# Kernel optimization log

Hardware: AMD Instinct MI355X
Metric: run time of the kernel (lower is better)

Reference implementation:

```python
import jax, jax.numpy as jnp
import numpy as np

N = 50000
T = 6
E = 800000
F_IN = 64
HID = 64
HEADS = 4
NEG_SLOPE = 0.2
BN_EPS = 1e-5


def _gat_layer(x, src, dst, W, att_src, att_dst, bias, concat):
    # x: [N, Fin]; W: [Fin, H*C]; att_*: [H, C]; src/dst: [E+N] (self loops appended)
    n = x.shape[0]
    H, C = att_src.shape
    xl = (x @ W).reshape(n, H, C)                     # [N, H, C]
    a_src = jnp.sum(xl * att_src[None], axis=-1)      # [N, H]
    a_dst = jnp.sum(xl * att_dst[None], axis=-1)      # [N, H]
    e = jax.nn.leaky_relu(a_src[src] + a_dst[dst], NEG_SLOPE)  # [E', H]
    # segment softmax over destination nodes (every node has a self loop)
    m = jax.ops.segment_max(e, dst, num_segments=n)
    ex = jnp.exp(e - m[dst])
    s = jax.ops.segment_sum(ex, dst, num_segments=n)
    alpha = ex / (s[dst] + 1e-16)                     # [E', H]
    msg = alpha[:, :, None] * xl[src]                 # [E', H, C]
    out = jax.ops.segment_sum(msg, dst, num_segments=n)  # [N, H, C]
    if concat:
        out = out.reshape(n, H * C)
    else:
        out = out.mean(axis=1)
    return out + bias


def _forward(x_seq, edge_index, W1, as1, ad1, b1, W2, as2, ad2, b2,
             cw1, cb1, g1, be1, cw2, cb2, g2, be2, lw1, lb1, lw2, lb2):
    n = x_seq.shape[1]
    self_loop = jnp.arange(n, dtype=edge_index.dtype)
    src = jnp.concatenate([edge_index[0], self_loop])
    dst = jnp.concatenate([edge_index[1], self_loop])

    def per_t(x):
        h = _gat_layer(x, src, dst, W1, as1, ad1, b1, concat=True)
        h = jax.nn.elu(h)
        h = _gat_layer(h, src, dst, W2, as2, ad2, b2, concat=False)
        h = jax.nn.elu(h)
        return h                                      # [N, HID]

    temporal = jax.vmap(per_t)(x_seq)                 # [T, N, HID]
    temporal = jnp.transpose(temporal, (1, 2, 0))     # [N, HID, T]

    def conv_bn_relu(t, cw, cb, g, be):
        y = jax.lax.conv_general_dilated(
            t, cw, window_strides=(1,), padding=[(1, 1)],
            dimension_numbers=('NCH', 'OIH', 'NCH')) + cb[None, :, None]
        # BatchNorm1d in eval mode, running_mean=0, running_var=1
        y = y * (g / jnp.sqrt(1.0 + BN_EPS))[None, :, None] + be[None, :, None]
        return jax.nn.relu(y)

    t = conv_bn_relu(temporal, cw1, cb1, g1, be1)
    t = conv_bn_relu(t, cw2, cb2, g2, be2)
    pooled = t.mean(axis=-1)                          # adaptive avg pool -> [N, HID]
    h = jax.nn.relu(pooled @ lw1 + lb1)
    logits = h @ lw2 + lb2                            # [N, 1]
    return logits


def setup_inputs() -> dict:
    key = jax.random.key(0)
    ks = jax.random.split(key, 20)
    C1 = HID // HEADS  # 16
    s = 0.1
    return {
        'x_seq': jax.random.normal(ks[0], (T, N, F_IN), jnp.float32),
        'edge_index': jax.random.randint(ks[1], (2, E), 0, N, jnp.int32),
        'W1': jax.random.normal(ks[2], (F_IN, HEADS * C1), jnp.float32) * s,
        'as1': jax.random.normal(ks[3], (HEADS, C1), jnp.float32) * s,
        'ad1': jax.random.normal(ks[4], (HEADS, C1), jnp.float32) * s,
        'b1': jnp.zeros((HEADS * C1,), jnp.float32),
        'W2': jax.random.normal(ks[5], (HID, HEADS * HID), jnp.float32) * s,
        'as2': jax.random.normal(ks[6], (HEADS, HID), jnp.float32) * s,
        'ad2': jax.random.normal(ks[7], (HEADS, HID), jnp.float32) * s,
        'b2': jnp.zeros((HID,), jnp.float32),
        'cw1': jax.random.normal(ks[8], (HID, HID, 3), jnp.float32) * s,
        'cb1': jnp.zeros((HID,), jnp.float32),
        'g1': jnp.ones((HID,), jnp.float32),
        'be1': jnp.zeros((HID,), jnp.float32),
        'cw2': jax.random.normal(ks[9], (HID, HID, 3), jnp.float32) * s,
        'cb2': jnp.zeros((HID,), jnp.float32),
        'g2': jnp.ones((HID,), jnp.float32),
        'be2': jnp.zeros((HID,), jnp.float32),
        'lw1': jax.random.normal(ks[10], (HID, HID // 2), jnp.float32) * s,
        'lb1': jnp.zeros((HID // 2,), jnp.float32),
        'lw2': jax.random.normal(ks[11], (HID // 2, 1), jnp.float32) * s,
        'lb2': jnp.zeros((1,), jnp.float32),
    }


def reference(x_seq, edge_index, W1, as1, ad1, b1, W2, as2, ad2, b2,
              cw1, cb1, g1, be1, cw2, cb2, g2, be2, lw1, lb1, lw2, lb2):
    return _forward(x_seq, edge_index, W1, as1, ad1, b1, W2, as2, ad2, b2,
                    cw1, cb1, g1, be1, cw2, cb2, g2, be2, lw1, lb1, lw2, lb2)
```

## Files before the change

kernel.cpp:

```cpp
#include <hip/hip_runtime.h>
#include <math.h>

#define NN 50000
#define EE 800000
#define TT 6

__device__ __forceinline__ float lrelu(float x){ return x > 0.f ? x : 0.2f*x; }
__device__ __forceinline__ float eluf(float x){ return x > 0.f ? x : expm1f(x); }

__global__ void k_init_counts(int* __restrict__ c){
  int i = blockIdx.x*256 + threadIdx.x;
  if (i < NN) c[i] = 1;
}

__global__ void k_hist(const int* __restrict__ dst, int* __restrict__ c){
  int i = blockIdx.x*256 + threadIdx.x;
  if (i < EE) atomicAdd(&c[dst[i]], 1);
}

__global__ void k_scanA(const int* __restrict__ cnt, int* __restrict__ excl,
                        int* __restrict__ bsum){
  __shared__ int sh[1024];
  int tid = threadIdx.x;
  int i = blockIdx.x*1024 + tid;
  int v = (i < NN) ? cnt[i] : 0;
  int x = v;
  sh[tid] = x; __syncthreads();
  for (int off = 1; off < 1024; off <<= 1){
    int y = (tid >= off) ? sh[tid - off] : 0;
    __syncthreads();
    x += y; sh[tid] = x; __syncthreads();
  }
  if (i < NN) excl[i] = x - v;
  if (tid == 1023) bsum[blockIdx.x] = x;
}

__global__ void k_scanB(int* __restrict__ bsum, int nb){
  if (threadIdx.x == 0){
    int run = 0;
    for (int b = 0; b < nb; ++b){ int t = bsum[b]; bsum[b] = run; run += t; }
  }
}

__global__ void k_scanC(const int* __restrict__ excl, const int* __restrict__ bsum,
                        int* __restrict__ rowptr, int* __restrict__ cursor){
  int i = blockIdx.x*1024 + threadIdx.x;
  if (i < NN){
    int v = excl[i] + bsum[blockIdx.x];
    rowptr[i] = v; cursor[i] = v;
  }
  if (i == 0) rowptr[NN] = EE + NN;
}

__global__ void k_scatter(const int* __restrict__ ei, int* __restrict__ cursor,
                          int* __restrict__ csr){
  int i = blockIdx.x*256 + threadIdx.x;
  if (i < EE){
    int d = ei[EE + i];
    int p = atomicAdd(&cursor[d], 1);
    csr[p] = ei[i];
  } else if (i < EE + NN){
    int v = i - EE;
    int p = atomicAdd(&cursor[v], 1);
    csr[p] = v;
  }
}

__global__ void k_prep(const float* __restrict__ W1, const float* __restrict__ as1,
                       const float* __restrict__ ad1,
                       const float* __restrict__ W2, const float* __restrict__ as2,
                       const float* __restrict__ ad2,
                       const float* __restrict__ cw1, const float* __restrict__ cw2,
                       const float* __restrict__ lw1,
                       float* __restrict__ Was1, float* __restrict__ Wad1,
                       float* __restrict__ Wat2, float* __restrict__ Wb,
                       float4* __restrict__ wq1, float4* __restrict__ wq2,
                       float* __restrict__ lw1t){
  int tid = threadIdx.x;
  int k = tid >> 2, h = tid & 3;
  float s1 = 0.f, d1 = 0.f, s2 = 0.f, d2 = 0.f;
  for (int c = 0; c < 16; ++c){
    float w = W1[k*64 + h*16 + c];
    s1 += w * as1[h*16 + c];
    d1 += w * ad1[h*16 + c];
  }
  for (int c = 0; c < 64; ++c){
    float w = W2[k*256 + h*64 + c];
    s2 += w * as2[h*64 + c];
    d2 += w * ad2[h*64 + c];
  }
  Was1[k*4+h] = s1; Wad1[k*4+h] = d1;
  Wat2[k*8 + h] = s2; Wat2[k*8 + 4 + h] = d2;
  for (int idx = tid; idx < 256*64; idx += 256){
    int kf = idx >> 6, c = idx & 63;
    int hh = kf >> 6, kk = kf & 63;
    Wb[idx] = W2[kk*256 + hh*64 + c];
  }
  for (int idx = tid; idx < 64*64; idx += 256){
    int o = idx >> 6, i = idx & 63;
    wq1[idx] = make_float4(cw1[o*192+i*3], cw1[o*192+i*3+1], cw1[o*192+i*3+2], 0.f);
    wq2[idx] = make_float4(cw2[o*192+i*3], cw2[o*192+i*3+1], cw2[o*192+i*3+2], 0.f);
  }
  for (int idx = tid; idx < 32*64; idx += 256){
    int j = idx >> 6, kk = idx & 63;
    lw1t[idx] = lw1[kk*32 + j];
  }
}

__global__ __launch_bounds__(256) void k_gemm_att1(const float* __restrict__ A,
                            const float* __restrict__ W,
                            const float* __restrict__ Was, const float* __restrict__ Wad,
                            float* __restrict__ Xl, float* __restrict__ a_src,
                            float* __restrict__ a_dst){
  __shared__ float At[64][16];
  int tid = threadIdx.x;
  int r0 = blockIdx.x * 16;
  {
    const float4* A4 = (const float4*)(A + (size_t)r0*64);
    float4 v = A4[tid];
    int r = tid >> 4, k4 = (tid & 15) << 2;
    At[k4+0][r] = v.x; At[k4+1][r] = v.y;
    At[k4+2][r] = v.z; At[k4+3][r] = v.w;
  }
  __syncthreads();
  int col = tid & 63;
  int rbase = (tid >> 6) << 2;
  float acc0=0.f, acc1=0.f, acc2=0.f, acc3=0.f;
  for (int k = 0; k < 64; ++k){
    float w = W[k*64 + col];
    float4 a4 = *(const float4*)&At[k][rbase];
    acc0 += a4.x*w; acc1 += a4.y*w; acc2 += a4.z*w; acc3 += a4.w*w;
  }
  Xl[(size_t)(r0+rbase+0)*64 + col] = acc0;
  Xl[(size_t)(r0+rbase+1)*64 + col] = acc1;
  Xl[(size_t)(r0+rbase+2)*64 + col] = acc2;
  Xl[(size_t)(r0+rbase+3)*64 + col] = acc3;
  if (tid < 128){
    int r = tid >> 3, jx = tid & 7;
    int h = jx & 3;
    const float* Wv = (jx < 4) ? Was : Wad;
    float a = 0.f;
    for (int k = 0; k < 64; ++k) a += At[k][r] * Wv[k*4 + h];
    if (jx < 4) a_src[(r0 + r)*4 + h] = a;
    else        a_dst[(r0 + r)*4 + h] = a;
  }
}

__global__ void k_agg1(const float* __restrict__ xl, const float* __restrict__ a_src,
                       const float* __restrict__ a_dst, const float* __restrict__ b1,
                       const float* __restrict__ Wat2,
                       const int* __restrict__ rowptr, const int* __restrict__ csr,
                       float* __restrict__ h1,
                       float* __restrict__ a_src2, float* __restrict__ a_dst2){
  int lane = threadIdx.x & 63;
  int wid  = threadIdx.x >> 6;
  int n = blockIdx.x*4 + wid;
  int h = lane >> 4;
  float ad = a_dst[n*4 + h];
  int rs = rowptr[n], re = rowptr[n+1];
  float s = 0.f, acc = 0.f;
  int j = rs;
  for (; j + 4 <= re; j += 4){
    int sn0=csr[j], sn1=csr[j+1], sn2=csr[j+2], sn3=csr[j+3];
    float e0=a_src[sn0*4+h], e1=a_src[sn1*4+h], e2=a_src[sn2*4+h], e3=a_src[sn3*4+h];
    float x0=xl[(size_t)sn0*64+lane], x1=xl[(size_t)sn1*64+lane];
    float x2=xl[(size_t)sn2*64+lane], x3=xl[(size_t)sn3*64+lane];
    float p0=__expf(lrelu(e0+ad)), p1=__expf(lrelu(e1+ad));
    float p2=__expf(lrelu(e2+ad)), p3=__expf(lrelu(e3+ad));
    s += p0; acc += p0*x0;
    s += p1; acc += p1*x1;
    s += p2; acc += p2*x2;
    s += p3; acc += p3*x3;
  }
  for (; j < re; ++j){
    int sn = csr[j];
    float p = __expf(lrelu(a_src[sn*4+h] + ad));
    float x = xl[(size_t)sn*64 + lane];
    s += p; acc += p*x;
  }
  float hv = eluf(acc/(s + 1e-16f) + b1[lane]);
  h1[(size_t)n*64 + lane] = hv;
  float4 wA = ((const float4*)Wat2)[lane*2];
  float4 wB = ((const float4*)Wat2)[lane*2 + 1];
  float p[8];
  p[0]=hv*wA.x; p[1]=hv*wA.y; p[2]=hv*wA.z; p[3]=hv*wA.w;
  p[4]=hv*wB.x; p[5]=hv*wB.y; p[6]=hv*wB.z; p[7]=hv*wB.w;
#pragma unroll
  for (int off = 32; off >= 1; off >>= 1){
#pragma unroll
    for (int q = 0; q < 8; ++q) p[q] += __shfl_xor(p[q], off);
  }
  if (lane == 0){
    ((float4*)a_src2)[n] = make_float4(p[0],p[1],p[2],p[3]);
    ((float4*)a_dst2)[n] = make_float4(p[4],p[5],p[6],p[7]);
  }
}

__global__ void k_agg2(const float* __restrict__ h1, const float* __restrict__ a_src,
                       const float* __restrict__ a_dst,
                       const int* __restrict__ rowptr, const int* __restrict__ csr,
                       float* __restrict__ agg){
  int lane = threadIdx.x & 63;
  int wid  = threadIdx.x >> 6;
  int n = blockIdx.x*4 + wid;
  float4 ad = ((const float4*)a_dst)[n];
  int rs = rowptr[n], re = rowptr[n+1];
  float s0=0.f,s1=0.f,s2=0.f,s3=0.f;
  float g0=0.f,g1=0.f,g2=0.f,g3=0.f;
  int j = rs;
  for (; j + 4 <= re; j += 4){
    int sa=csr[j], sb=csr[j+1], sc=csr[j+2], sd=csr[j+3];
    float4 ea = ((const float4*)a_src)[sa];
    float4 eb = ((const float4*)a_src)[sb];
    float4 ec = ((const float4*)a_src)[sc];
    float4 ed = ((const float4*)a_src)[sd];
    float xa = h1[(size_t)sa*64 + lane];
    float xb = h1[(size_t)sb*64 + lane];
    float xc = h1[(size_t)sc*64 + lane];
    float xd = h1[(size_t)sd*64 + lane];
    float pa0=__expf(lrelu(ea.x+ad.x)), pa1=__expf(lrelu(ea.y+ad.y));
    float pa2=__expf(lrelu(ea.z+ad.z)), pa3=__expf(lrelu(ea.w+ad.w));
    float pb0=__expf(lrelu(eb.x+ad.x)), pb1=__expf(lrelu(eb.y+ad.y));
    float pb2=__expf(lrelu(eb.z+ad.z)), pb3=__expf(lrelu(eb.w+ad.w));
    float pc0=__expf(lrelu(ec.x+ad.x)), pc1=__expf(lrelu(ec.y+ad.y));
    float pc2=__expf(lrelu(ec.z+ad.z)), pc3=__expf(lrelu(ec.w+ad.w));
    float pd0=__expf(lrelu(ed.x+ad.x)), pd1=__expf(lrelu(ed.y+ad.y));
    float pd2=__expf(lrelu(ed.z+ad.z)), pd3=__expf(lrelu(ed.w+ad.w));
    s0 += pa0+pb0+pc0+pd0; g0 += pa0*xa + pb0*xb + pc0*xc + pd0*xd;
    s1 += pa1+pb1+pc1+pd1; g1 += pa1*xa + pb1*xb + pc1*xc + pd1*xd;
    s2 += pa2+pb2+pc2+pd2; g2 += pa2*xa + pb2*xb + pc2*xc + pd2*xd;
    s3 += pa3+pb3+pc3+pd3; g3 += pa3*xa + pb3*xb + pc3*xc + pd3*xd;
  }
  for (; j < re; ++j){
    int sn = csr[j];
    float4 ev = ((const float4*)a_src)[sn];
    float x = h1[(size_t)sn*64 + lane];
    float p0=__expf(lrelu(ev.x+ad.x)), p1=__expf(lrelu(ev.y+ad.y));
    float p2=__expf(lrelu(ev.z+ad.z)), p3=__expf(lrelu(ev.w+ad.w));
    s0 += p0; g0 += p0*x;
    s1 += p1; g1 += p1*x;
    s2 += p2; g2 += p2*x;
    s3 += p3; g3 += p3*x;
  }
  size_t base = (size_t)n*256 + lane;
  agg[base      ] = g0/(s0 + 1e-16f);
  agg[base +  64] = g1/(s1 + 1e-16f);
  agg[base + 128] = g2/(s2 + 1e-16f);
  agg[base + 192] = g3/(s3 + 1e-16f);
}

__global__ __launch_bounds__(256) void k_out2(const float* __restrict__ agg,
                                              const float* __restrict__ Wb,
                                              const float* __restrict__ b2,
                                              float* __restrict__ Xq, int t){
  __shared__ float AtF[256*20];
  int tid = threadIdx.x;
  int r0 = blockIdx.x * 16;
  const float4* A4 = (const float4*)(agg + (size_t)r0*256);
#pragma unroll
  for (int jj = 0; jj < 4; ++jj){
    int m = tid + 256*jj;
    float4 v = A4[m];
    int row = m >> 6, k0 = (m & 63) << 2;
    AtF[(k0+0)*20 + row] = v.x;
    AtF[(k0+1)*20 + row] = v.y;
    AtF[(k0+2)*20 + row] = v.z;
    AtF[(k0+3)*20 + row] = v.w;
  }
  __syncthreads();
  int col = tid & 63;
  int rbase = (tid >> 6) << 2;
  float acc0=0.f, acc1=0.f, acc2=0.f, acc3=0.f;
  for (int k = 0; k < 256; ++k){
    float w = Wb[(size_t)k*64 + col];
    float4 a4 = *(const float4*)&AtF[k*20 + rbase];
    acc0 += a4.x*w; acc1 += a4.y*w; acc2 += a4.z*w; acc3 += a4.w*w;
  }
  float bb = b2[col];
  float4 v = make_float4(eluf(0.25f*acc0 + bb), eluf(0.25f*acc1 + bb),
                         eluf(0.25f*acc2 + bb), eluf(0.25f*acc3 + bb));
  *(float4*)(Xq + ((size_t)col*6 + t)*NN + (r0 + rbase)) = v;
}

__global__ __launch_bounds__(256) void k_conv1(const float* __restrict__ Xq,
    float* __restrict__ C1,
    const float4* __restrict__ wq1, const float* __restrict__ cb1,
    const float* __restrict__ g1,   const float* __restrict__ be1){
  int lane = threadIdx.x & 63;
  int w = __builtin_amdgcn_readfirstlane(threadIdx.x >> 6);
  int n = blockIdx.x*64 + lane;
  int nc = (n < NN) ? n : (NN-1);
  int ob = w*16;
  float acc[16][6];
#pragma unroll
  for (int o = 0; o < 16; ++o){
    float c = cb1[ob+o];
#pragma unroll
    for (int t = 0; t < 6; ++t) acc[o][t] = c;
  }
  for (int i = 0; i < 64; ++i){
    const float* xp = Xq + (size_t)i*6*NN + nc;
    float x1 = xp[0], x2 = xp[NN], x3 = xp[2*(size_t)NN];
    float x4 = xp[3*(size_t)NN], x5 = xp[4*(size_t)NN], x6 = xp[5*(size_t)NN];
#pragma unroll
    for (int o = 0; o < 16; ++o){
      float4 wv = wq1[(ob+o)*64 + i];
      acc[o][0] += wv.y*x1 + wv.z*x2;
      acc[o][1] += wv.x*x1 + wv.y*x2 + wv.z*x3;
      acc[o][2] += wv.x*x2 + wv.y*x3 + wv.z*x4;
      acc[o][3] += wv.x*x3 + wv.y*x4 + wv.z*x5;
      acc[o][4] += wv.x*x4 + wv.y*x5 + wv.z*x6;
      acc[o][5] += wv.x*x5 + wv.y*x6;
    }
  }
  if (n < NN){
#pragma unroll
    for (int o = 0; o < 16; ++o){
      float bns = g1[ob+o]*rsqrtf(1.f + 1e-5f), be = be1[ob+o];
      float* cp = C1 + (size_t)(ob+o)*6*NN + n;
#pragma unroll
      for (int t = 0; t < 6; ++t) cp[(size_t)t*NN] = fmaxf(acc[o][t]*bns + be, 0.f);
    }
  }
}

__global__ __launch_bounds__(256) void k_conv2(const float* __restrict__ C1,
    const float4* __restrict__ wq2, const float* __restrict__ cb2,
    const float* __restrict__ g2,   const float* __restrict__ be2,
    const float* __restrict__ lw1t, const float* __restrict__ lb1,
    const float* __restrict__ lw2,  const float* __restrict__ lb2,
    float* __restrict__ out){
  __shared__ float pool_lds[64][65];
  __shared__ float outp[4][64];
  int lane = threadIdx.x & 63;
  int w = __builtin_amdgcn_readfirstlane(threadIdx.x >> 6);
  int n = blockIdx.x*64 + lane;
  int nc = (n < NN) ? n : (NN-1);
  int ob = w*16;
  float acc[16][6];
#pragma unroll
  for (int o = 0; o < 16; ++o){
    float c = cb2[ob+o];
#pragma unroll
    for (int t = 0; t < 6; ++t) acc[o][t] = c;
  }
  for (int i = 0; i < 64; ++i){
    const float* xp = C1 + (size_t)i*6*NN + nc;
    float x1 = xp[0], x2 = xp[NN], x3 = xp[2*(size_t)NN];
    float x4 = xp[3*(size_t)NN], x5 = xp[4*(size_t)NN], x6 = xp[5*(size_t)NN];
#pragma unroll
    for (int o = 0; o < 16; ++o){
      float4 wv = wq2[(ob+o)*64 + i];
      acc[o][0] += wv.y*x1 + wv.z*x2;
      acc[o][1] += wv.x*x1 + wv.y*x2 + wv.z*x3;
      acc[o][2] += wv.x*x2 + wv.y*x3 + wv.z*x4;
      acc[o][3] += wv.x*x3 + wv.y*x4 + wv.z*x5;
      acc[o][4] += wv.x*x4 + wv.y*x5 + wv.z*x6;
      acc[o][5] += wv.x*x5 + wv.y*x6;
    }
  }
#pragma unroll
  for (int o = 0; o < 16; ++o){
    float bns = g2[ob+o]*rsqrtf(1.f + 1e-5f), be = be2[ob+o];
    float pooled = 0.f;
#pragma unroll
    for (int t = 0; t < 6; ++t) pooled += fmaxf(acc[o][t]*bns + be, 0.f);
    pool_lds[ob+o][lane] = pooled*(1.f/6.f);
  }
  __syncthreads();
  {
    float hacc[8];
#pragma unroll
    for (int jj = 0; jj < 8; ++jj) hacc[jj] = 0.f;
    for (int k = 0; k < 64; ++k){
      float pk = pool_lds[k][lane];
#pragma unroll
      for (int jj = 0; jj < 8; ++jj)
        hacc[jj] += pk * lw1t[(w*8+jj)*64 + k];
    }
    float po = 0.f;
#pragma unroll
    for (int jj = 0; jj < 8; ++jj)
      po += fmaxf(hacc[jj] + lb1[w*8+jj], 0.f) * lw2[w*8+jj];
    outp[w][lane] = po;
  }
  __syncthreads();
  if (w == 0 && n < NN)
    out[n] = outp[0][lane] + outp[1][lane] + outp[2][lane] + outp[3][lane] + lb2[0];
}

extern "C" void kernel_launch(void* const* d_in, const int* in_sizes, int n_in,
                              void* d_out, int out_size, void* d_ws, size_t ws_size,
                              hipStream_t stream) {
  const float* x_seq = (const float*)d_in[0];
  const int*   ei    = (const int*)  d_in[1];
  const float* W1  = (const float*)d_in[2];
  const float* as1 = (const float*)d_in[3];
  const float* ad1 = (const float*)d_in[4];
  const float* b1  = (const float*)d_in[5];
  const float* W2  = (const float*)d_in[6];
  const float* as2 = (const float*)d_in[7];
  const float* ad2 = (const float*)d_in[8];
  const float* b2  = (const float*)d_in[9];
  const float* cw1 = (const float*)d_in[10];
  const float* cb1 = (const float*)d_in[11];
  const float* g1  = (const float*)d_in[12];
  const float* be1 = (const float*)d_in[13];
  const float* cw2 = (const float*)d_in[14];
  const float* cb2 = (const float*)d_in[15];
  const float* g2  = (const float*)d_in[16];
  const float* be2 = (const float*)d_in[17];
  const float* lw1 = (const float*)d_in[18];
  const float* lb1 = (const float*)d_in[19];
  const float* lw2 = (const float*)d_in[20];
  const float* lb2 = (const float*)d_in[21];
  float* out = (float*)d_out;

  const size_t QSZ = (size_t)64*6*NN*sizeof(float);
  char* wp = (char*)d_ws;
  auto alloc = [&](size_t bytes) -> char* {
    char* p = wp; wp += (bytes + 255) & ~(size_t)255; return p;
  };
  char* region1 = alloc(QSZ);
  float* Xq = (float*)alloc(QSZ);
  float* Was1 = (float*)alloc(256*sizeof(float));
  float* Wad1 = (float*)alloc(256*sizeof(float));
  float* Wat2 = (float*)alloc(64*8*sizeof(float));
  float* Wb   = (float*)alloc(256*64*sizeof(float));
  float4* wq1 = (float4*)alloc(64*64*sizeof(float4));
  float4* wq2 = (float4*)alloc(64*64*sizeof(float4));
  float* lw1t = (float*)alloc(32*64*sizeof(float));

  char* sp = region1;
  auto salloc = [&](size_t bytes) -> char* {
    char* p = sp; sp += (bytes + 255) & ~(size_t)255; return p;
  };
  int*   counts = (int*)  salloc(NN*sizeof(int));
  int*   excl   = (int*)  salloc(NN*sizeof(int));
  int*   bsum   = (int*)  salloc(64*sizeof(int));
  int*   rowptr = (int*)  salloc((NN+1)*sizeof(int));
  int*   cursor = (int*)  salloc(NN*sizeof(int));
  int*   csr    = (int*)  salloc((size_t)(EE+NN)*sizeof(int));
  float* a_src1 = (float*)salloc((size_t)NN*4*sizeof(float));
  float* a_dst1 = (float*)salloc((size_t)NN*4*sizeof(float));
  float* a_src2 = (float*)salloc((size_t)NN*4*sizeof(float));
  float* a_dst2 = (float*)salloc((size_t)NN*4*sizeof(float));
  float* h1     = (float*)salloc((size_t)NN*64*sizeof(float));
  float* agg    = (float*)salloc((size_t)NN*256*sizeof(float));
  float* xl1    = agg;
  float* C1     = (float*)region1;

  const int NBSCAN = (NN + 1023)/1024;
  k_init_counts<<<(NN+255)/256, 256, 0, stream>>>(counts);
  k_hist<<<(EE+255)/256, 256, 0, stream>>>(ei + EE, counts);
  k_scanA<<<NBSCAN, 1024, 0, stream>>>(counts, excl, bsum);
  k_scanB<<<1, 64, 0, stream>>>(bsum, NBSCAN);
  k_scanC<<<NBSCAN, 1024, 0, stream>>>(excl, bsum, rowptr, cursor);
  k_scatter<<<(EE+NN+255)/256, 256, 0, stream>>>(ei, cursor, csr);
  k_prep<<<1, 256, 0, stream>>>(W1, as1, ad1, W2, as2, ad2, cw1, cw2, lw1,
                                Was1, Wad1, Wat2, Wb, wq1, wq2, lw1t);

  for (int t = 0; t < TT; ++t){
    const float* xt = x_seq + (size_t)t*NN*64;
    k_gemm_att1<<<NN/16, 256, 0, stream>>>(xt, W1, Was1, Wad1, xl1, a_src1, a_dst1);
    k_agg1<<<NN/4, 256, 0, stream>>>(xl1, a_src1, a_dst1, b1, Wat2, rowptr, csr,
                                     h1, a_src2, a_dst2);
    k_agg2<<<NN/4, 256, 0, stream>>>(h1, a_src2, a_dst2, rowptr, csr, agg);
    k_out2<<<NN/16, 256, 0, stream>>>(agg, Wb, b2, Xq, t);
  }
  const int NB64 = (NN + 63)/64;
  k_conv1<<<NB64, 256, 0, stream>>>(Xq, C1, wq1, cb1, g1, be1);
  k_conv2<<<NB64, 256, 0, stream>>>(C1, wq2, cb2, g2, be2,
                                    lw1t, lb1, lw2, lb2, out);
}
```

Measured before the change: 1.450 ms.

## Split edge aggregation across two waves, widen conv grids, stage out2 stores, separate MLP

The two GAT aggregation kernels now assign two wavefronts to each destination node, splitting the edge list by parity and combining the partial sums through shared memory. This is meant to cut per-wave serial latency on high-degree nodes. The conv kernels are split across twice as many blocks, eight output channels per wave instead of sixteen, to raise occupancy. The MLP head moves out of conv2 into its own kernel, which costs a global round trip through a new pooled buffer. k_out2 transposes its results through LDS so that the global stores into the [channel][t][node] layout are coalesced.

Result: slower. 1.532 ms (+5.7%).

```diff
diff --git a/kernel.cpp b/kernel.cpp
--- a/kernel.cpp
+++ b/kernel.cpp
@@ -146,22 +146,27 @@
   }
 }
 
-__global__ void k_agg1(const float* __restrict__ xl, const float* __restrict__ a_src,
+__global__ __launch_bounds__(256) void k_agg1(
+                       const float* __restrict__ xl, const float* __restrict__ a_src,
                        const float* __restrict__ a_dst, const float* __restrict__ b1,
                        const float* __restrict__ Wat2,
                        const int* __restrict__ rowptr, const int* __restrict__ csr,
                        float* __restrict__ h1,
                        float* __restrict__ a_src2, float* __restrict__ a_dst2){
+  __shared__ float gpart[2][64];
+  __shared__ float spart[2][64];
   int lane = threadIdx.x & 63;
   int wid  = threadIdx.x >> 6;
-  int n = blockIdx.x*4 + wid;
+  int nl   = wid >> 1;
+  int half = wid & 1;
+  int n = blockIdx.x*2 + nl;
   int h = lane >> 4;
   float ad = a_dst[n*4 + h];
   int rs = rowptr[n], re = rowptr[n+1];
   float s = 0.f, acc = 0.f;
-  int j = rs;
-  for (; j + 4 <= re; j += 4){
-    int sn0=csr[j], sn1=csr[j+1], sn2=csr[j+2], sn3=csr[j+3];
+  int j = rs + half;
+  for (; j + 6 < re; j += 8){
+    int sn0=csr[j], sn1=csr[j+2], sn2=csr[j+4], sn3=csr[j+6];
     float e0=a_src[sn0*4+h], e1=a_src[sn1*4+h], e2=a_src[sn2*4+h], e3=a_src[sn3*4+h];
     float x0=xl[(size_t)sn0*64+lane], x1=xl[(size_t)sn1*64+lane];
     float x2=xl[(size_t)sn2*64+lane], x3=xl[(size_t)sn3*64+lane];
@@ -172,44 +177,55 @@
     s += p2; acc += p2*x2;
     s += p3; acc += p3*x3;
   }
-  for (; j < re; ++j){
+  for (; j < re; j += 2){
     int sn = csr[j];
     float p = __expf(lrelu(a_src[sn*4+h] + ad));
     float x = xl[(size_t)sn*64 + lane];
     s += p; acc += p*x;
   }
-  float hv = eluf(acc/(s + 1e-16f) + b1[lane]);
-  h1[(size_t)n*64 + lane] = hv;
-  float4 wA = ((const float4*)Wat2)[lane*2];
-  float4 wB = ((const float4*)Wat2)[lane*2 + 1];
-  float p[8];
-  p[0]=hv*wA.x; p[1]=hv*wA.y; p[2]=hv*wA.z; p[3]=hv*wA.w;
-  p[4]=hv*wB.x; p[5]=hv*wB.y; p[6]=hv*wB.z; p[7]=hv*wB.w;
-#pragma unroll
-  for (int off = 32; off >= 1; off >>= 1){
-#pragma unroll
-    for (int q = 0; q < 8; ++q) p[q] += __shfl_xor(p[q], off);
-  }
-  if (lane == 0){
-    ((float4*)a_src2)[n] = make_float4(p[0],p[1],p[2],p[3]);
-    ((float4*)a_dst2)[n] = make_float4(p[4],p[5],p[6],p[7]);
-  }
-}
-
-__global__ void k_agg2(const float* __restrict__ h1, const float* __restrict__ a_src,
+  if (half == 1){ gpart[nl][lane] = acc; spart[nl][lane] = s; }
+  __syncthreads();
+  if (half == 0){
+    acc += gpart[nl][lane];
+    s   += spart[nl][lane];
+    float hv = eluf(acc/(s + 1e-16f) + b1[lane]);
+    h1[(size_t)n*64 + lane] = hv;
+    float4 wA = ((const float4*)Wat2)[lane*2];
+    float4 wB = ((const float4*)Wat2)[lane*2 + 1];
+    float p[8];
+    p[0]=hv*wA.x; p[1]=hv*wA.y; p[2]=hv*wA.z; p[3]=hv*wA.w;
+    p[4]=hv*wB.x; p[5]=hv*wB.y; p[6]=hv*wB.z; p[7]=hv*wB.w;
+#pragma unroll
+    for (int off = 32; off >= 1; off >>= 1){
+#pragma unroll
+      for (int q = 0; q < 8; ++q) p[q] += __shfl_xor(p[q], off);
+    }
+    if (lane == 0){
+      ((float4*)a_src2)[n] = make_float4(p[0],p[1],p[2],p[3]);
+      ((float4*)a_dst2)[n] = make_float4(p[4],p[5],p[6],p[7]);
+    }
+  }
+}
+
+__global__ __launch_bounds__(256) void k_agg2(
+                       const float* __restrict__ h1, const float* __restrict__ a_src,
                        const float* __restrict__ a_dst,
                        const int* __restrict__ rowptr, const int* __restrict__ csr,
                        float* __restrict__ agg){
+  __shared__ float gpart[2][4][64];
+  __shared__ float4 spart[2];
   int lane = threadIdx.x & 63;
   int wid  = threadIdx.x >> 6;
-  int n = blockIdx.x*4 + wid;
+  int nl   = wid >> 1;
+  int half = wid & 1;
+  int n = blockIdx.x*2 + nl;
   float4 ad = ((const float4*)a_dst)[n];
   int rs = rowptr[n], re = rowptr[n+1];
   float s0=0.f,s1=0.f,s2=0.f,s3=0.f;
   float g0=0.f,g1=0.f,g2=0.f,g3=0.f;
-  int j = rs;
-  for (; j + 4 <= re; j += 4){
-    int sa=csr[j], sb=csr[j+1], sc=csr[j+2], sd=csr[j+3];
+  int j = rs + half;
+  for (; j + 6 < re; j += 8){
+    int sa=csr[j], sb=csr[j+2], sc=csr[j+4], sd=csr[j+6];
     float4 ea = ((const float4*)a_src)[sa];
     float4 eb = ((const float4*)a_src)[sb];
     float4 ec = ((const float4*)a_src)[sc];
@@ -231,7 +247,7 @@
     s2 += pa2+pb2+pc2+pd2; g2 += pa2*xa + pb2*xb + pc2*xc + pd2*xd;
     s3 += pa3+pb3+pc3+pd3; g3 += pa3*xa + pb3*xb + pc3*xc + pd3*xd;
   }
-  for (; j < re; ++j){
+  for (; j < re; j += 2){
     int sn = csr[j];
     float4 ev = ((const float4*)a_src)[sn];
     float x = h1[(size_t)sn*64 + lane];
@@ -242,11 +258,24 @@
     s2 += p2; g2 += p2*x;
     s3 += p3; g3 += p3*x;
   }
-  size_t base = (size_t)n*256 + lane;
-  agg[base      ] = g0/(s0 + 1e-16f);
-  agg[base +  64] = g1/(s1 + 1e-16f);
-  agg[base + 128] = g2/(s2 + 1e-16f);
-  agg[base + 192] = g3/(s3 + 1e-16f);
+  if (half == 1){
+    gpart[nl][0][lane] = g0; gpart[nl][1][lane] = g1;
+    gpart[nl][2][lane] = g2; gpart[nl][3][lane] = g3;
+    if (lane == 0) spart[nl] = make_float4(s0,s1,s2,s3);
+  }
+  __syncthreads();
+  if (half == 0){
+    float4 sp = spart[nl];
+    g0 += gpart[nl][0][lane]; s0 += sp.x;
+    g1 += gpart[nl][1][lane]; s1 += sp.y;
+    g2 += gpart[nl][2][lane]; s2 += sp.z;
+    g3 += gpart[nl][3][lane]; s3 += sp.w;
+    size_t base = (size_t)n*256 + lane;
+    agg[base      ] = g0/(s0 + 1e-16f);
+    agg[base +  64] = g1/(s1 + 1e-16f);
+    agg[base + 128] = g2/(s2 + 1e-16f);
+    agg[base + 192] = g3/(s3 + 1e-16f);
+  }
 }
 
 __global__ __launch_bounds__(256) void k_out2(const float* __restrict__ agg,
@@ -277,9 +306,16 @@
     acc0 += a4.x*w; acc1 += a4.y*w; acc2 += a4.z*w; acc3 += a4.w*w;
   }
   float bb = b2[col];
-  float4 v = make_float4(eluf(0.25f*acc0 + bb), eluf(0.25f*acc1 + bb),
-                         eluf(0.25f*acc2 + bb), eluf(0.25f*acc3 + bb));
-  *(float4*)(Xq + ((size_t)col*6 + t)*NN + (r0 + rbase)) = v;
+  __syncthreads();
+  AtF[col*17 + rbase+0] = eluf(0.25f*acc0 + bb);
+  AtF[col*17 + rbase+1] = eluf(0.25f*acc1 + bb);
+  AtF[col*17 + rbase+2] = eluf(0.25f*acc2 + bb);
+  AtF[col*17 + rbase+3] = eluf(0.25f*acc3 + bb);
+  __syncthreads();
+  int ch = tid >> 2, q = tid & 3;
+  float4 ov = make_float4(AtF[ch*17 + q*4+0], AtF[ch*17 + q*4+1],
+                          AtF[ch*17 + q*4+2], AtF[ch*17 + q*4+3]);
+  *(float4*)(Xq + ((size_t)ch*6 + t)*NN + r0 + q*4) = ov;
 }
 
 __global__ __launch_bounds__(256) void k_conv1(const float* __restrict__ Xq,
@@ -288,12 +324,13 @@
     const float* __restrict__ g1,   const float* __restrict__ be1){
   int lane = threadIdx.x & 63;
   int w = __builtin_amdgcn_readfirstlane(threadIdx.x >> 6);
-  int n = blockIdx.x*64 + lane;
+  int bb = blockIdx.x;
+  int n = (bb >> 1)*64 + lane;
   int nc = (n < NN) ? n : (NN-1);
-  int ob = w*16;
-  float acc[16][6];
-#pragma unroll
-  for (int o = 0; o < 16; ++o){
+  int ob = (bb & 1)*32 + w*8;
+  float acc[8][6];
+#pragma unroll
+  for (int o = 0; o < 8; ++o){
     float c = cb1[ob+o];
 #pragma unroll
     for (int t = 0; t < 6; ++t) acc[o][t] = c;
@@ -303,7 +340,7 @@
     float x1 = xp[0], x2 = xp[NN], x3 = xp[2*(size_t)NN];
     float x4 = xp[3*(size_t)NN], x5 = xp[4*(size_t)NN], x6 = xp[5*(size_t)NN];
 #pragma unroll
-    for (int o = 0; o < 16; ++o){
+    for (int o = 0; o < 8; ++o){
       float4 wv = wq1[(ob+o)*64 + i];
       acc[o][0] += wv.y*x1 + wv.z*x2;
       acc[o][1] += wv.x*x1 + wv.y*x2 + wv.z*x3;
@@ -315,7 +352,7 @@
   }
   if (n < NN){
 #pragma unroll
-    for (int o = 0; o < 16; ++o){
+    for (int o = 0; o < 8; ++o){
       float bns = g1[ob+o]*rsqrtf(1.f + 1e-5f), be = be1[ob+o];
       float* cp = C1 + (size_t)(ob+o)*6*NN + n;
 #pragma unroll
@@ -327,19 +364,16 @@
 __global__ __launch_bounds__(256) void k_conv2(const float* __restrict__ C1,
     const float4* __restrict__ wq2, const float* __restrict__ cb2,
     const float* __restrict__ g2,   const float* __restrict__ be2,
-    const float* __restrict__ lw1t, const float* __restrict__ lb1,
-    const float* __restrict__ lw2,  const float* __restrict__ lb2,
-    float* __restrict__ out){
-  __shared__ float pool_lds[64][65];
-  __shared__ float outp[4][64];
+    float* __restrict__ pooledG){
   int lane = threadIdx.x & 63;
   int w = __builtin_amdgcn_readfirstlane(threadIdx.x >> 6);
-  int n = blockIdx.x*64 + lane;
+  int bb = blockIdx.x;
+  int n = (bb >> 1)*64 + lane;
   int nc = (n < NN) ? n : (NN-1);
-  int ob = w*16;
-  float acc[16][6];
-#pragma unroll
-  for (int o = 0; o < 16; ++o){
+  int ob = (bb & 1)*32 + w*8;
+  float acc[8][6];
+#pragma unroll
+  for (int o = 0; o < 8; ++o){
     float c = cb2[ob+o];
 #pragma unroll
     for (int t = 0; t < 6; ++t) acc[o][t] = c;
@@ -349,7 +383,7 @@
     float x1 = xp[0], x2 = xp[NN], x3 = xp[2*(size_t)NN];
     float x4 = xp[3*(size_t)NN], x5 = xp[4*(size_t)NN], x6 = xp[5*(size_t)NN];
 #pragma unroll
-    for (int o = 0; o < 16; ++o){
+    for (int o = 0; o < 8; ++o){
       float4 wv = wq2[(ob+o)*64 + i];
       acc[o][0] += wv.y*x1 + wv.z*x2;
       acc[o][1] += wv.x*x1 + wv.y*x2 + wv.z*x3;
@@ -359,34 +393,37 @@
       acc[o][5] += wv.x*x5 + wv.y*x6;
     }
   }
-#pragma unroll
-  for (int o = 0; o < 16; ++o){
-    float bns = g2[ob+o]*rsqrtf(1.f + 1e-5f), be = be2[ob+o];
-    float pooled = 0.f;
-#pragma unroll
-    for (int t = 0; t < 6; ++t) pooled += fmaxf(acc[o][t]*bns + be, 0.f);
-    pool_lds[ob+o][lane] = pooled*(1.f/6.f);
-  }
-  __syncthreads();
-  {
-    float hacc[8];
-#pragma unroll
-    for (int jj = 0; jj < 8; ++jj) hacc[jj] = 0.f;
-    for (int k = 0; k < 64; ++k){
-      float pk = pool_lds[k][lane];
-#pragma unroll
-      for (int jj = 0; jj < 8; ++jj)
-        hacc[jj] += pk * lw1t[(w*8+jj)*64 + k];
+  if (n < NN){
+#pragma unroll
+    for (int o = 0; o < 8; ++o){
+      float bns = g2[ob+o]*rsqrtf(1.f + 1e-5f), be = be2[ob+o];
+      float pooled = 0.f;
+#pragma unroll
+      for (int t = 0; t < 6; ++t) pooled += fmaxf(acc[o][t]*bns + be, 0.f);
+      pooledG[(size_t)(ob+o)*NN + n] = pooled*(1.f/6.f);
     }
-    float po = 0.f;
-#pragma unroll
-    for (int jj = 0; jj < 8; ++jj)
-      po += fmaxf(hacc[jj] + lb1[w*8+jj], 0.f) * lw2[w*8+jj];
-    outp[w][lane] = po;
-  }
-  __syncthreads();
-  if (w == 0 && n < NN)
-    out[n] = outp[0][lane] + outp[1][lane] + outp[2][lane] + outp[3][lane] + lb2[0];
+  }
+}
+
+__global__ __launch_bounds__(256) void k_mlp(const float* __restrict__ pooledG,
+    const float* __restrict__ lw1t, const float* __restrict__ lb1,
+    const float* __restrict__ lw2,  const float* __restrict__ lb2,
+    float* __restrict__ out){
+  int lane = threadIdx.x & 63;
+  int w = __builtin_amdgcn_readfirstlane(threadIdx.x >> 6);
+  int n = (blockIdx.x*4 + w)*64 + lane;
+  int nc = (n < NN) ? n : (NN-1);
+  float p[64];
+#pragma unroll 16
+  for (int o = 0; o < 64; ++o) p[o] = pooledG[(size_t)o*NN + nc];
+  float po = 0.f;
+  for (int j = 0; j < 32; ++j){
+    float hj = lb1[j];
+#pragma unroll 16
+    for (int k = 0; k < 64; ++k) hj += p[k] * lw1t[j*64 + k];
+    po += fmaxf(hj, 0.f) * lw2[j];
+  }
+  if (n < NN) out[n] = po + lb2[0];
 }
 
 extern "C" void kernel_launch(void* const* d_in, const int* in_sizes, int n_in,
@@ -423,6 +460,7 @@
   };
   char* region1 = alloc(QSZ);
   float* Xq = (float*)alloc(QSZ);
+  float* pooledG = (float*)alloc((size_t)64*NN*sizeof(float));
   float* Was1 = (float*)alloc(256*sizeof(float));
   float* Wad1 = (float*)alloc(256*sizeof(float));
   float* Wat2 = (float*)alloc(64*8*sizeof(float));
@@ -463,13 +501,13 @@
   for (int t = 0; t < TT; ++t){
     const float* xt = x_seq + (size_t)t*NN*64;
     k_gemm_att1<<<NN/16, 256, 0, stream>>>(xt, W1, Was1, Wad1, xl1, a_src1, a_dst1);
-    k_agg1<<<NN/4, 256, 0, stream>>>(xl1, a_src1, a_dst1, b1, Wat2, rowptr, csr,
+    k_agg1<<<NN/2, 256, 0, stream>>>(xl1, a_src1, a_dst1, b1, Wat2, rowptr, csr,
                                      h1, a_src2, a_dst2);
-    k_agg2<<<NN/4, 256, 0, stream>>>(h1, a_src2, a_dst2, rowptr, csr, agg);
+    k_agg2<<<NN/2, 256, 0, stream>>>(h1, a_src2, a_dst2, rowptr, csr, agg);
     k_out2<<<NN/16, 256, 0, stream>>>(agg, Wb, b2, Xq, t);
   }
   const int NB64 = (NN + 63)/64;
-  k_conv1<<<NB64, 256, 0, stream>>>(Xq, C1, wq1, cb1, g1, be1);
-  k_conv2<<<NB64, 256, 0, stream>>>(C1, wq2, cb2, g2, be2,
-                                    lw1t, lb1, lw2, lb2, out);
-}
+  k_conv1<<<NB64*2, 256, 0, stream>>>(Xq, C1, wq1, cb1, g1, be1);
+  k_conv2<<<NB64*2, 256, 0, stream>>>(C1, wq2, cb2, g2, be2, pooledG);
+  k_mlp<<<(NN+255)/256, 256, 0, stream>>>(pooledG, lw1t, lb1, lw2, lb2, out);
+}
```

## Fuse both temporal convs via LDS tile, split MLP, unroll aggregation loops by eight

Applied to the files above, without the earlier changes.

The two edge-aggregation loops are unrolled from four to eight neighbours and given launch bounds, so more gathers are in flight per wave. k_out2 now writes node-major rows per timestep instead of a transposed channel-time layout. conv1 and conv2 are merged into one kernel that stages a 32-node tile of all channels and timesteps in LDS and keeps the conv1 result there, which avoids writing and rereading the C1 intermediate. The final MLP moves to a separate kernel that reads a pooled buffer. In exchange there is one extra kernel launch and a pooled round trip through global memory, and the larger unroll may raise register pressure.

New measurement: 1.554 ms, median of 3. 7.1% more time.

```diff
diff --git a/kernel.cpp b/kernel.cpp
--- a/kernel.cpp
+++ b/kernel.cpp
@@ -146,7 +146,8 @@
   }
 }
 
-__global__ void k_agg1(const float* __restrict__ xl, const float* __restrict__ a_src,
+__global__ __launch_bounds__(256) void k_agg1(
+                       const float* __restrict__ xl, const float* __restrict__ a_src,
                        const float* __restrict__ a_dst, const float* __restrict__ b1,
                        const float* __restrict__ Wat2,
                        const int* __restrict__ rowptr, const int* __restrict__ csr,
@@ -160,17 +161,27 @@
   int rs = rowptr[n], re = rowptr[n+1];
   float s = 0.f, acc = 0.f;
   int j = rs;
-  for (; j + 4 <= re; j += 4){
-    int sn0=csr[j], sn1=csr[j+1], sn2=csr[j+2], sn3=csr[j+3];
+  for (; j + 8 <= re; j += 8){
+    int sn0=csr[j],   sn1=csr[j+1], sn2=csr[j+2], sn3=csr[j+3];
+    int sn4=csr[j+4], sn5=csr[j+5], sn6=csr[j+6], sn7=csr[j+7];
     float e0=a_src[sn0*4+h], e1=a_src[sn1*4+h], e2=a_src[sn2*4+h], e3=a_src[sn3*4+h];
+    float e4=a_src[sn4*4+h], e5=a_src[sn5*4+h], e6=a_src[sn6*4+h], e7=a_src[sn7*4+h];
     float x0=xl[(size_t)sn0*64+lane], x1=xl[(size_t)sn1*64+lane];
     float x2=xl[(size_t)sn2*64+lane], x3=xl[(size_t)sn3*64+lane];
+    float x4=xl[(size_t)sn4*64+lane], x5=xl[(size_t)sn5*64+lane];
+    float x6=xl[(size_t)sn6*64+lane], x7=xl[(size_t)sn7*64+lane];
     float p0=__expf(lrelu(e0+ad)), p1=__expf(lrelu(e1+ad));
     float p2=__expf(lrelu(e2+ad)), p3=__expf(lrelu(e3+ad));
+    float p4=__expf(lrelu(e4+ad)), p5=__expf(lrelu(e5+ad));
+    float p6=__expf(lrelu(e6+ad)), p7=__expf(lrelu(e7+ad));
     s += p0; acc += p0*x0;
     s += p1; acc += p1*x1;
     s += p2; acc += p2*x2;
     s += p3; acc += p3*x3;
+    s += p4; acc += p4*x4;
+    s += p5; acc += p5*x5;
+    s += p6; acc += p6*x6;
+    s += p7; acc += p7*x7;
   }
   for (; j < re; ++j){
     int sn = csr[j];
@@ -196,7 +207,8 @@
   }
 }
 
-__global__ void k_agg2(const float* __restrict__ h1, const float* __restrict__ a_src,
+__global__ __launch_bounds__(256) void k_agg2(
+                       const float* __restrict__ h1, const float* __restrict__ a_src,
                        const float* __restrict__ a_dst,
                        const int* __restrict__ rowptr, const int* __restrict__ csr,
                        float* __restrict__ agg){
@@ -208,16 +220,25 @@
   float s0=0.f,s1=0.f,s2=0.f,s3=0.f;
   float g0=0.f,g1=0.f,g2=0.f,g3=0.f;
   int j = rs;
-  for (; j + 4 <= re; j += 4){
-    int sa=csr[j], sb=csr[j+1], sc=csr[j+2], sd=csr[j+3];
+  for (; j + 8 <= re; j += 8){
+    int sa=csr[j],   sb=csr[j+1], sc=csr[j+2], sd=csr[j+3];
+    int se=csr[j+4], sf=csr[j+5], sg=csr[j+6], sh=csr[j+7];
     float4 ea = ((const float4*)a_src)[sa];
     float4 eb = ((const float4*)a_src)[sb];
     float4 ec = ((const float4*)a_src)[sc];
     float4 ed = ((const float4*)a_src)[sd];
+    float4 ee = ((const float4*)a_src)[se];
+    float4 ef = ((const float4*)a_src)[sf];
+    float4 eg = ((const float4*)a_src)[sg];
+    float4 eh = ((const float4*)a_src)[sh];
     float xa = h1[(size_t)sa*64 + lane];
     float xb = h1[(size_t)sb*64 + lane];
     float xc = h1[(size_t)sc*64 + lane];
     float xd = h1[(size_t)sd*64 + lane];
+    float xe = h1[(size_t)se*64 + lane];
+    float xf = h1[(size_t)sf*64 + lane];
+    float xg = h1[(size_t)sg*64 + lane];
+    float xh = h1[(size_t)sh*64 + lane];
     float pa0=__expf(lrelu(ea.x+ad.x)), pa1=__expf(lrelu(ea.y+ad.y));
     float pa2=__expf(lrelu(ea.z+ad.z)), pa3=__expf(lrelu(ea.w+ad.w));
     float pb0=__expf(lrelu(eb.x+ad.x)), pb1=__expf(lrelu(eb.y+ad.y));
@@ -226,10 +247,22 @@
     float pc2=__expf(lrelu(ec.z+ad.z)), pc3=__expf(lrelu(ec.w+ad.w));
     float pd0=__expf(lrelu(ed.x+ad.x)), pd1=__expf(lrelu(ed.y+ad.y));
     float pd2=__expf(lrelu(ed.z+ad.z)), pd3=__expf(lrelu(ed.w+ad.w));
-    s0 += pa0+pb0+pc0+pd0; g0 += pa0*xa + pb0*xb + pc0*xc + pd0*xd;
-    s1 += pa1+pb1+pc1+pd1; g1 += pa1*xa + pb1*xb + pc1*xc + pd1*xd;
-    s2 += pa2+pb2+pc2+pd2; g2 += pa2*xa + pb2*xb + pc2*xc + pd2*xd;
-    s3 += pa3+pb3+pc3+pd3; g3 += pa3*xa + pb3*xb + pc3*xc + pd3*xd;
+    float pe0=__expf(lrelu(ee.x+ad.x)), pe1=__expf(lrelu(ee.y+ad.y));
+    float pe2=__expf(lrelu(ee.z+ad.z)), pe3=__expf(lrelu(ee.w+ad.w));
+    float pf0=__expf(lrelu(ef.x+ad.x)), pf1=__expf(lrelu(ef.y+ad.y));
+    float pf2=__expf(lrelu(ef.z+ad.z)), pf3=__expf(lrelu(ef.w+ad.w));
+    float pg0=__expf(lrelu(eg.x+ad.x)), pg1=__expf(lrelu(eg.y+ad.y));
+    float pg2=__expf(lrelu(eg.z+ad.z)), pg3=__expf(lrelu(eg.w+ad.w));
+    float ph0=__expf(lrelu(eh.x+ad.x)), ph1=__expf(lrelu(eh.y+ad.y));
+    float ph2=__expf(lrelu(eh.z+ad.z)), ph3=__expf(lrelu(eh.w+ad.w));
+    s0 += pa0+pb0+pc0+pd0+pe0+pf0+pg0+ph0;
+    g0 += pa0*xa + pb0*xb + pc0*xc + pd0*xd + pe0*xe + pf0*xf + pg0*xg + ph0*xh;
+    s1 += pa1+pb1+pc1+pd1+pe1+pf1+pg1+ph1;
+    g1 += pa1*xa + pb1*xb + pc1*xc + pd1*xd + pe1*xe + pf1*xf + pg1*xg + ph1*xh;
+    s2 += pa2+pb2+pc2+pd2+pe2+pf2+pg2+ph2;
+    g2 += pa2*xa + pb2*xb + pc2*xc + pd2*xd + pe2*xe + pf2*xf + pg2*xg + ph2*xh;
+    s3 += pa3+pb3+pc3+pd3+pe3+pf3+pg3+ph3;
+    g3 += pa3*xa + pb3*xb + pc3*xc + pd3*xd + pe3*xe + pf3*xf + pg3*xg + ph3*xh;
   }
   for (; j < re; ++j){
     int sn = csr[j];
@@ -252,7 +285,7 @@
 __global__ __launch_bounds__(256) void k_out2(const float* __restrict__ agg,
                                               const float* __restrict__ Wb,
                                               const float* __restrict__ b2,
-                                              float* __restrict__ Xq, int t){
+                                              float* __restrict__ ht){
   __shared__ float AtF[256*20];
   int tid = threadIdx.x;
   int r0 = blockIdx.x * 16;
@@ -277,33 +310,54 @@
     acc0 += a4.x*w; acc1 += a4.y*w; acc2 += a4.z*w; acc3 += a4.w*w;
   }
   float bb = b2[col];
-  float4 v = make_float4(eluf(0.25f*acc0 + bb), eluf(0.25f*acc1 + bb),
-                         eluf(0.25f*acc2 + bb), eluf(0.25f*acc3 + bb));
-  *(float4*)(Xq + ((size_t)col*6 + t)*NN + (r0 + rbase)) = v;
-}
-
-__global__ __launch_bounds__(256) void k_conv1(const float* __restrict__ Xq,
-    float* __restrict__ C1,
+  ht[(size_t)(r0+rbase+0)*64 + col] = eluf(0.25f*acc0 + bb);
+  ht[(size_t)(r0+rbase+1)*64 + col] = eluf(0.25f*acc1 + bb);
+  ht[(size_t)(r0+rbase+2)*64 + col] = eluf(0.25f*acc2 + bb);
+  ht[(size_t)(r0+rbase+3)*64 + col] = eluf(0.25f*acc3 + bb);
+}
+
+__global__ __launch_bounds__(256) void k_conv(const float* __restrict__ htb,
     const float4* __restrict__ wq1, const float* __restrict__ cb1,
-    const float* __restrict__ g1,   const float* __restrict__ be1){
-  int lane = threadIdx.x & 63;
-  int w = __builtin_amdgcn_readfirstlane(threadIdx.x >> 6);
-  int n = blockIdx.x*64 + lane;
-  int nc = (n < NN) ? n : (NN-1);
-  int ob = w*16;
-  float acc[16][6];
-#pragma unroll
-  for (int o = 0; o < 16; ++o){
+    const float* __restrict__ g1,   const float* __restrict__ be1,
+    const float4* __restrict__ wq2, const float* __restrict__ cb2,
+    const float* __restrict__ g2,   const float* __restrict__ be2,
+    float* __restrict__ pooledG){
+  __shared__ float X[64*198];
+  int tid  = threadIdx.x;
+  int lane = tid & 63;
+  int w    = __builtin_amdgcn_readfirstlane(tid >> 6);
+  int nn   = lane & 31;
+  int half = lane >> 5;
+  int n0 = blockIdx.x*32;
+  int n  = n0 + nn;
+  int ob = w*16 + half*8;
+
+#pragma unroll
+  for (int k = 0; k < 8; ++k){
+    int p  = k*256 + tid;
+    int ch = p & 63, ns = p >> 6;
+    int nsrc = n0 + ns; if (nsrc >= NN) nsrc = NN-1;
+    float xv[6];
+#pragma unroll
+    for (int t = 0; t < 6; ++t) xv[t] = htb[((size_t)t*NN + nsrc)*64 + ch];
+#pragma unroll
+    for (int t = 0; t < 6; ++t) X[ch*198 + t*33 + ns] = xv[t];
+  }
+  __syncthreads();
+
+  float acc[8][6];
+#pragma unroll
+  for (int o = 0; o < 8; ++o){
     float c = cb1[ob+o];
 #pragma unroll
     for (int t = 0; t < 6; ++t) acc[o][t] = c;
   }
   for (int i = 0; i < 64; ++i){
-    const float* xp = Xq + (size_t)i*6*NN + nc;
-    float x1 = xp[0], x2 = xp[NN], x3 = xp[2*(size_t)NN];
-    float x4 = xp[3*(size_t)NN], x5 = xp[4*(size_t)NN], x6 = xp[5*(size_t)NN];
-#pragma unroll
-    for (int o = 0; o < 16; ++o){
+    const float* xp = X + i*198 + nn;
+    float x1 = xp[0], x2 = xp[33], x3 = xp[66];
+    float x4 = xp[99], x5 = xp[132], x6 = xp[165];
+#pragma unroll
+    for (int o = 0; o < 8; ++o){
       float4 wv = wq1[(ob+o)*64 + i];
       acc[o][0] += wv.y*x1 + wv.z*x2;
       acc[o][1] += wv.x*x1 + wv.y*x2 + wv.z*x3;
@@ -313,43 +367,28 @@
       acc[o][5] += wv.x*x5 + wv.y*x6;
     }
   }
-  if (n < NN){
-#pragma unroll
-    for (int o = 0; o < 16; ++o){
-      float bns = g1[ob+o]*rsqrtf(1.f + 1e-5f), be = be1[ob+o];
-      float* cp = C1 + (size_t)(ob+o)*6*NN + n;
-#pragma unroll
-      for (int t = 0; t < 6; ++t) cp[(size_t)t*NN] = fmaxf(acc[o][t]*bns + be, 0.f);
-    }
-  }
-}
-
-__global__ __launch_bounds__(256) void k_conv2(const float* __restrict__ C1,
-    const float4* __restrict__ wq2, const float* __restrict__ cb2,
-    const float* __restrict__ g2,   const float* __restrict__ be2,
-    const float* __restrict__ lw1t, const float* __restrict__ lb1,
-    const float* __restrict__ lw2,  const float* __restrict__ lb2,
-    float* __restrict__ out){
-  __shared__ float pool_lds[64][65];
-  __shared__ float outp[4][64];
-  int lane = threadIdx.x & 63;
-  int w = __builtin_amdgcn_readfirstlane(threadIdx.x >> 6);
-  int n = blockIdx.x*64 + lane;
-  int nc = (n < NN) ? n : (NN-1);
-  int ob = w*16;
-  float acc[16][6];
-#pragma unroll
-  for (int o = 0; o < 16; ++o){
+  __syncthreads();
+#pragma unroll
+  for (int o = 0; o < 8; ++o){
+    float bns = g1[ob+o]*rsqrtf(1.f + 1e-5f), be = be1[ob+o];
+    float* xp = X + (ob+o)*198 + nn;
+#pragma unroll
+    for (int t = 0; t < 6; ++t) xp[t*33] = fmaxf(acc[o][t]*bns + be, 0.f);
+  }
+  __syncthreads();
+
+#pragma unroll
+  for (int o = 0; o < 8; ++o){
     float c = cb2[ob+o];
 #pragma unroll
     for (int t = 0; t < 6; ++t) acc[o][t] = c;
   }
   for (int i = 0; i < 64; ++i){
-    const float* xp = C1 + (size_t)i*6*NN + nc;
-    float x1 = xp[0], x2 = xp[NN], x3 = xp[2*(size_t)NN];
-    float x4 = xp[3*(size_t)NN], x5 = xp[4*(size_t)NN], x6 = xp[5*(size_t)NN];
-#pragma unroll
-    for (int o = 0; o < 16; ++o){
+    const float* xp = X + i*198 + nn;
+    float x1 = xp[0], x2 = xp[33], x3 = xp[66];
+    float x4 = xp[99], x5 = xp[132], x6 = xp[165];
+#pragma unroll
+    for (int o = 0; o < 8; ++o){
       float4 wv = wq2[(ob+o)*64 + i];
       acc[o][0] += wv.y*x1 + wv.z*x2;
       acc[o][1] += wv.x*x1 + wv.y*x2 + wv.z*x3;
@@ -359,34 +398,37 @@
       acc[o][5] += wv.x*x5 + wv.y*x6;
     }
   }
-#pragma unroll
-  for (int o = 0; o < 16; ++o){
-    float bns = g2[ob+o]*rsqrtf(1.f + 1e-5f), be = be2[ob+o];
-    float pooled = 0.f;
-#pragma unroll
-    for (int t = 0; t < 6; ++t) pooled += fmaxf(acc[o][t]*bns + be, 0.f);
-    pool_lds[ob+o][lane] = pooled*(1.f/6.f);
-  }
-  __syncthreads();
-  {
-    float hacc[8];
-#pragma unroll
-    for (int jj = 0; jj < 8; ++jj) hacc[jj] = 0.f;
-    for (int k = 0; k < 64; ++k){
-      float pk = pool_lds[k][lane];
-#pragma unroll
-      for (int jj = 0; jj < 8; ++jj)
-        hacc[jj] += pk * lw1t[(w*8+jj)*64 + k];
+  if (n < NN){
+#pragma unroll
+    for (int o = 0; o < 8; ++o){
+      float bns = g2[ob+o]*rsqrtf(1.f + 1e-5f), be = be2[ob+o];
+      float pooled = 0.f;
+#pragma unroll
+      for (int t = 0; t < 6; ++t) pooled += fmaxf(acc[o][t]*bns + be, 0.f);
+      pooledG[(size_t)(ob+o)*NN + n] = pooled*(1.f/6.f);
     }
-    float po = 0.f;
-#pragma unroll
-    for (int jj = 0; jj < 8; ++jj)
-      po += fmaxf(hacc[jj] + lb1[w*8+jj], 0.f) * lw2[w*8+jj];
-    outp[w][lane] = po;
-  }
-  __syncthreads();
-  if (w == 0 && n < NN)
-    out[n] = outp[0][lane] + outp[1][lane] + outp[2][lane] + outp[3][lane] + lb2[0];
+  }
+}
+
+__global__ __launch_bounds__(256) void k_mlp(const float* __restrict__ pooledG,
+    const float* __restrict__ lw1t, const float* __restrict__ lb1,
+    const float* __restrict__ lw2,  const float* __restrict__ lb2,
+    float* __restrict__ out){
+  int lane = threadIdx.x & 63;
+  int w = __builtin_amdgcn_readfirstlane(threadIdx.x >> 6);
+  int n = (blockIdx.x*4 + w)*64 + lane;
+  int nc = (n < NN) ? n : (NN-1);
+  float p[64];
+#pragma unroll 16
+  for (int o = 0; o < 64; ++o) p[o] = pooledG[(size_t)o*NN + nc];
+  float po = 0.f;
+  for (int j = 0; j < 32; ++j){
+    float hj = lb1[j];
+#pragma unroll 16
+    for (int k = 0; k < 64; ++k) hj += p[k] * lw1t[j*64 + k];
+    po += fmaxf(hj, 0.f) * lw2[j];
+  }
+  if (n < NN) out[n] = po + lb2[0];
 }
 
 extern "C" void kernel_launch(void* const* d_in, const int* in_sizes, int n_in,
@@ -416,13 +458,25 @@
   const float* lb2 = (const float*)d_in[21];
   float* out = (float*)d_out;
 
-  const size_t QSZ = (size_t)64*6*NN*sizeof(float);
   char* wp = (char*)d_ws;
   auto alloc = [&](size_t bytes) -> char* {
     char* p = wp; wp += (bytes + 255) & ~(size_t)255; return p;
   };
-  char* region1 = alloc(QSZ);
-  float* Xq = (float*)alloc(QSZ);
+  int*   counts = (int*)  alloc(NN*sizeof(int));
+  int*   excl   = (int*)  alloc(NN*sizeof(int));
+  int*   bsum   = (int*)  alloc(64*sizeof(int));
+  int*   rowptr = (int*)  alloc((NN+1)*sizeof(int));
+  int*   cursor = (int*)  alloc(NN*sizeof(int));
+  int*   csr    = (int*)  alloc((size_t)(EE+NN)*sizeof(int));
+  float* a_src1 = (float*)alloc((size_t)NN*4*sizeof(float));
+  float* a_dst1 = (float*)alloc((size_t)NN*4*sizeof(float));
+  float* a_src2 = (float*)alloc((size_t)NN*4*sizeof(float));
+  float* a_dst2 = (float*)alloc((size_t)NN*4*sizeof(float));
+  float* h1     = (float*)alloc((size_t)NN*64*sizeof(float));
+  float* agg    = (float*)alloc((size_t)NN*256*sizeof(float));
+  float* xl1    = agg;
+  float* htb    = (float*)alloc((size_t)TT*NN*64*sizeof(float));
+  float* pooledG= (float*)alloc((size_t)64*NN*sizeof(float));
   float* Was1 = (float*)alloc(256*sizeof(float));
   float* Wad1 = (float*)alloc(256*sizeof(float));
   float* Wat2 = (float*)alloc(64*8*sizeof(float));
@@ -430,25 +484,6 @@
   float4* wq1 = (float4*)alloc(64*64*sizeof(float4));
   float4* wq2 = (float4*)alloc(64*64*sizeof(float4));
   float* lw1t = (float*)alloc(32*64*sizeof(float));
-
-  char* sp = region1;
-  auto salloc = [&](size_t bytes) -> char* {
-    char* p = sp; sp += (bytes + 255) & ~(size_t)255; return p;
-  };
-  int*   counts = (int*)  salloc(NN*sizeof(int));
-  int*   excl   = (int*)  salloc(NN*sizeof(int));
-  int*   bsum   = (int*)  salloc(64*sizeof(int));
-  int*   rowptr = (int*)  salloc((NN+1)*sizeof(int));
-  int*   cursor = (int*)  salloc(NN*sizeof(int));
-  int*   csr    = (int*)  salloc((size_t)(EE+NN)*sizeof(int));
-  float* a_src1 = (float*)salloc((size_t)NN*4*sizeof(float));
-  float* a_dst1 = (float*)salloc((size_t)NN*4*sizeof(float));
-  float* a_src2 = (float*)salloc((size_t)NN*4*sizeof(float));
-  float* a_dst2 = (float*)salloc((size_t)NN*4*sizeof(float));
-  float* h1     = (float*)salloc((size_t)NN*64*sizeof(float));
-  float* agg    = (float*)salloc((size_t)NN*256*sizeof(float));
-  float* xl1    = agg;
-  float* C1     = (float*)region1;
 
   const int NBSCAN = (NN + 1023)/1024;
   k_init_counts<<<(NN+255)/256, 256, 0, stream>>>(counts);
@@ -466,10 +501,9 @@
     k_agg1<<<NN/4, 256, 0, stream>>>(xl1, a_src1, a_dst1, b1, Wat2, rowptr, csr,
                                      h1, a_src2, a_dst2);
     k_agg2<<<NN/4, 256, 0, stream>>>(h1, a_src2, a_dst2, rowptr, csr, agg);
-    k_out2<<<NN/16, 256, 0, stream>>>(agg, Wb, b2, Xq, t);
-  }
-  const int NB64 = (NN + 63)/64;
-  k_conv1<<<NB64, 256, 0, stream>>>(Xq, C1, wq1, cb1, g1, be1);
-  k_conv2<<<NB64, 256, 0, stream>>>(C1, wq2, cb2, g2, be2,
-                                    lw1t, lb1, lw2, lb2, out);
-}
+    k_out2<<<NN/16, 256, 0, stream>>>(agg, Wb, b2, htb + (size_t)t*NN*64);
+  }
+  k_conv<<<(NN+31)/32, 256, 0, stream>>>(htb, wq1, cb1, g1, be1, wq2, cb2, g2, be2,
+                                         pooledG);
+  k_mlp<<<(NN+255)/256, 256, 0, stream>>>(pooledG, lw1t, lb1, lw2, lb2, out);
+}
```
